# Kernel tuning notes

Hardware: AMD Instinct MI355X
Metric: run time of the kernel (lower is better)

The kernel has to match this reference:

```python
import jax, jax.numpy as jnp
import numpy as np

N, IN_DIM, H, K = 4096, 64, 64, 3
DT = 0.05


def graph_filter(z, S_powers, W):
    # z: [N, d_in], S_powers: [K, N, N], W: [K, d_in, d_out]
    zk = jnp.einsum('knm,md->knd', S_powers, z)   # K-hop diffused features
    return jnp.einsum('knd,kde->ne', zk, W)       # sum over taps k


def setup_inputs() -> dict:
    key = jax.random.key(0)
    ks = jax.random.split(key, 8)
    w_scale = 0.1
    return {
        'x': jax.random.normal(ks[0], (N, H), jnp.float32),
        'u': jax.random.normal(ks[1], (N, IN_DIM), jnp.float32),
        'S_powers': jax.random.normal(ks[2], (K, N, N), jnp.float32) / np.float32(np.sqrt(N)),
        'WA_hat': jax.random.normal(ks[3], (K, H, H), jnp.float32) * w_scale,
        'WB_hat': jax.random.normal(ks[4], (K, IN_DIM, H), jnp.float32) * w_scale,
        'WA_state': jax.random.normal(ks[5], (K, H, H), jnp.float32) * w_scale,
        'WB_state': jax.random.normal(ks[6], (K, IN_DIM, H), jnp.float32) * w_scale,
        'bx': jnp.zeros((1, H), jnp.float32),
        'bu': jnp.zeros((1, H), jnp.float32),
        'b': jnp.ones((1, H), jnp.float32) * 0.1,
        'n_steps': 4,
    }


def reference(x, u, S_powers, WA_hat, WB_hat, WA_state, WB_state, bx, bu, b, n_steps):
    # Input-driven terms are constant across solver steps; hoist them.
    fu = jax.nn.relu(graph_filter(u, S_powers, WB_hat) + bu)   # [N, H]
    sigma_c = jnp.tanh(graph_filter(u, S_powers, WB_state))    # [N, H]

    def step(xc, _):
        f = jax.nn.relu(graph_filter(xc, S_powers, WA_hat) + bx) + fu
        dx = -(b + f) * xc - graph_filter(xc, S_powers, WA_state) + f * sigma_c
        xn = jnp.clip(xc + DT * dx, -1.0, 1.0)
        return xn, None

    xf, _ = jax.lax.scan(step, x, None, length=n_steps)
    return xf
```

## Files before the change

kernel.cpp:

```cpp
#include <hip/hip_runtime.h>
#include <math.h>


typedef unsigned short u16;
typedef unsigned int u32;
typedef __attribute__((ext_vector_type(8))) short short8;
typedef __attribute__((ext_vector_type(4))) float f32x4;

#define NN 4096
#define HD 64
#define KB32 128
#define DT_C 0.05f

__device__ __forceinline__ u16 f2bf(float f) {
    u32 u = __float_as_uint(f);
    u += 0x7FFFu + ((u >> 16) & 1u);
    return (u16)(u >> 16);
}
__device__ __forceinline__ u32 pk2(float a, float b) {
    return (u32)f2bf(a) | ((u32)f2bf(b) << 16);
}

__global__ __launch_bounds__(256) void zprep_kernel(
    const float* __restrict__ u, const float* __restrict__ x,
    const float* __restrict__ WAh, const float* __restrict__ WAs,
    const float* __restrict__ WBh, const float* __restrict__ WBs,
    u16* __restrict__ utT, u16* __restrict__ xtT, u16* __restrict__ WtT)
{
    const int b = blockIdx.x;
    const int t = threadIdx.x;
    if (b < 256) {
        const float* z = (b < 128) ? u : x;
        u16* ztT = (b < 128) ? utT : xtT;
        const int kb = b & 127, n0 = kb * 32;
        __shared__ __align__(16) u16 tile[64][40];
        const int nl = t >> 3, c0 = (t & 7) * 8;
        const float* src = z + (size_t)(n0 + nl) * HD + c0;
        float4 f0 = ((const float4*)src)[0];
        float4 f1 = ((const float4*)src)[1];
        tile[c0 + 0][nl] = f2bf(f0.x); tile[c0 + 1][nl] = f2bf(f0.y);
        tile[c0 + 2][nl] = f2bf(f0.z); tile[c0 + 3][nl] = f2bf(f0.w);
        tile[c0 + 4][nl] = f2bf(f1.x); tile[c0 + 5][nl] = f2bf(f1.y);
        tile[c0 + 6][nl] = f2bf(f1.z); tile[c0 + 7][nl] = f2bf(f1.w);
        __syncthreads();
        const int e = t >> 2, kw0 = (t & 3) * 8;
        short8 v = *(const short8*)&tile[e][kw0];
        *(short8*)(ztT + ((size_t)kb * 64 + e) * 32 + kw0) = v;
    } else {
        for (int f = t; f < 4 * 6 * 64 * 32; f += 256) {
            int mat = f / 12288, r = f % 12288;
            int s = r / 2048, r2 = r % 2048;
            int e = r2 >> 5, kw = r2 & 31;
            int kp = s * 32 + kw, tap = kp >> 6, d = kp & 63;
            const float* Wm = (mat == 0) ? WAh : (mat == 1) ? WAs : (mat == 2) ? WBh : WBs;
            WtT[f] = f2bf(Wm[((size_t)tap * HD + d) * HD + e]);
        }
    }
}

__global__ __launch_bounds__(256) void diffuseA_kernel(
    const float* __restrict__ S, const u16* __restrict__ utT,
    const u16* __restrict__ xtT, u16* __restrict__ SbT,
    float* __restrict__ Yp, int iters)
{
    const int t = threadIdx.x;
    const int tap = blockIdx.z;
    const int row0 = blockIdx.x * 64;
    const int kb0 = blockIdx.y * iters;
    const int w = t >> 6, lane = t & 63, l15 = lane & 15, quad = lane >> 4;

    const int n = row0 + w * 16 + l15;
    const float* Sb = S + ((size_t)tap * NN + n) * NN + quad * 8;
    u16* Wb = SbT + (((size_t)tap * KB32) * NN + n) * 32 + quad * 8;

    f32x4 z4 = {0.f, 0.f, 0.f, 0.f};
    f32x4 acc[2][4];
    #pragma unroll
    for (int s = 0; s < 2; ++s)
        #pragma unroll
        for (int j = 0; j < 4; ++j) acc[s][j] = z4;

    #pragma unroll 2
    for (int it = 0; it < iters; ++it) {
        const int kb = kb0 + it;
        const float* sp0 = Sb + (size_t)kb * 32;
        float4 f0 = ((const float4*)sp0)[0];
        float4 f1 = ((const float4*)sp0)[1];
        short8 bu[4], bx[4];
        #pragma unroll
        for (int ct = 0; ct < 4; ++ct) {
            const size_t bo = ((size_t)kb * 64 + ct * 16 + l15) * 32 + quad * 8;
            bu[ct] = *(const short8*)(utT + bo);
            bx[ct] = *(const short8*)(xtT + bo);
        }
        union U { uint4 u4; short8 s8; };
        U A0;
        A0.u4.x = pk2(f0.x, f0.y); A0.u4.y = pk2(f0.z, f0.w);
        A0.u4.z = pk2(f1.x, f1.y); A0.u4.w = pk2(f1.z, f1.w);
        *(uint4*)(Wb + (size_t)kb * (NN * 32)) = A0.u4;
        #pragma unroll
        for (int ct = 0; ct < 4; ++ct) {
            acc[0][ct] = __builtin_amdgcn_mfma_f32_16x16x32_bf16(bu[ct], A0.s8, acc[0][ct], 0, 0, 0);
            acc[1][ct] = __builtin_amdgcn_mfma_f32_16x16x32_bf16(bx[ct], A0.s8, acc[1][ct], 0, 0, 0);
        }
    }
    #pragma unroll
    for (int s = 0; s < 2; ++s) {
        float* yb = Yp + ((size_t)((blockIdx.y * 3 + tap) * 2 + s) * NN + n) * HD + quad * 4;
        #pragma unroll
        for (int ct = 0; ct < 4; ++ct)
            *(f32x4*)(yb + ct * 16) = acc[s][ct];
    }
}

__global__ __launch_bounds__(256) void diffuseS_kernel(
    const u16* __restrict__ SbT, const u16* __restrict__ xtT,
    float* __restrict__ Yp, int iters)
{
    const int t = threadIdx.x;
    const int row0 = blockIdx.x * 64;
    const int kb0 = blockIdx.y * iters;
    const int w = t >> 6, lane = t & 63, l15 = lane & 15, quad = lane >> 4;

    const int n = row0 + w * 16 + l15;
    const u16* A0 = SbT + (size_t)n * 32 + quad * 8;
    const size_t kstr = (size_t)NN * 32;
    const size_t tstr = (size_t)KB32 * NN * 32;

    f32x4 z4 = {0.f, 0.f, 0.f, 0.f};
    f32x4 acc[3][4];
    #pragma unroll
    for (int tp = 0; tp < 3; ++tp)
        #pragma unroll
        for (int j = 0; j < 4; ++j) acc[tp][j] = z4;

    #pragma unroll 2
    for (int it = 0; it < iters; ++it) {
        const int kb = kb0 + it;
        short8 a[3];
        #pragma unroll
        for (int tp = 0; tp < 3; ++tp)
            a[tp] = *(const short8*)(A0 + (size_t)tp * tstr + (size_t)kb * kstr);
        short8 b[4];
        #pragma unroll
        for (int ct = 0; ct < 4; ++ct)
            b[ct] = *(const short8*)(xtT + ((size_t)kb * 64 + ct * 16 + l15) * 32 + quad * 8);
        #pragma unroll
        for (int tp = 0; tp < 3; ++tp)
            #pragma unroll
            for (int ct = 0; ct < 4; ++ct)
                acc[tp][ct] = __builtin_amdgcn_mfma_f32_16x16x32_bf16(b[ct], a[tp], acc[tp][ct], 0, 0, 0);
    }
    #pragma unroll
    for (int tp = 0; tp < 3; ++tp) {
        float* yb = Yp + ((size_t)(blockIdx.y * 3 + tp) * NN + n) * HD + quad * 4;
        #pragma unroll
        for (int ct = 0; ct < 4; ++ct)
            *(f32x4*)(yb + ct * 16) = acc[tp][ct];
    }
}

__global__ __launch_bounds__(256) void update_step_kernel(
    const float* __restrict__ Yp, int KS, const u16* __restrict__ WtT,
    const float* __restrict__ bx, const float* __restrict__ bvec,
    const float* __restrict__ fu, const float* __restrict__ sc,
    const float* __restrict__ xc, float* __restrict__ xn,
    u16* __restrict__ xtT, int do_pack)
{
    __shared__ __align__(16) u16 yt[6][16][56];
    __shared__ __align__(16) u16 pkt[64][24];
    const int t = threadIdx.x;
    const int n0 = blockIdx.x * 16;

    for (int f = t; f < 384; f += 256) {
        const int tap = f >> 7;
        const int r = f & 127;
        const int nl = r >> 3, d8 = r & 7, d0 = d8 * 8;
        const float* p = Yp + ((size_t)tap * NN + n0 + nl) * HD + d0;
        const size_t kstride = (size_t)3 * NN * HD;
        float4 s0 = {0.f, 0.f, 0.f, 0.f}, s1 = {0.f, 0.f, 0.f, 0.f};
        for (int y = 0; y < KS; ++y) {
            float4 v0 = ((const float4*)(p + (size_t)y * kstride))[0];
            float4 v1 = ((const float4*)(p + (size_t)y * kstride))[1];
            s0.x += v0.x; s0.y += v0.y; s0.z += v0.z; s0.w += v0.w;
            s1.x += v1.x; s1.y += v1.y; s1.z += v1.z; s1.w += v1.w;
        }
        uint4 o;
        o.x = pk2(s0.x, s0.y); o.y = pk2(s0.z, s0.w);
        o.z = pk2(s1.x, s1.y); o.w = pk2(s1.z, s1.w);
        const int s = tap * 2 + (d8 >> 2), kw0 = (d8 & 3) * 8;
        *(uint4*)&yt[s][nl][kw0] = o;
    }
    __syncthreads();

    const int wv = t >> 6, lane = t & 63, l15 = lane & 15, quad = lane >> 4;
    f32x4 z4 = {0.f, 0.f, 0.f, 0.f};
    f32x4 aF = z4, aG = z4;
    #pragma unroll
    for (int s = 0; s < 6; ++s) {
        short8 a = *(const short8*)&yt[s][l15][quad * 8];
        const size_t wo = ((size_t)s * 64 + wv * 16 + l15) * 32 + quad * 8;
        short8 bF = *(const short8*)(WtT + wo);
        short8 bG = *(const short8*)(WtT + wo + 12288);
        aF = __builtin_amdgcn_mfma_f32_16x16x32_bf16(a, bF, aF, 0, 0, 0);
        aG = __builtin_amdgcn_mfma_f32_16x16x32_bf16(a, bG, aG, 0, 0, 0);
    }
    const int e = wv * 16 + l15;
    const float bxv = bx[e], bbv = bvec[e];
    float xos[4];
    #pragma unroll
    for (int r = 0; r < 4; ++r) {
        const int n = n0 + quad * 4 + r;
        const size_t o = (size_t)n * HD + e;
        float ff = fmaxf(aF[r] + bxv, 0.f) + fu[o];
        float xv = xc[o];
        float dx = -(bbv + ff) * xv - aG[r] + ff * sc[o];
        float xo = fminf(fmaxf(xv + DT_C * dx, -1.f), 1.f);
        xn[o] = xo;
        xos[r] = xo;
    }
    if (do_pack) {
        uint2 pv;
        pv.x = pk2(xos[0], xos[1]);
        pv.y = pk2(xos[2], xos[3]);
        *(uint2*)&pkt[e][quad * 4] = pv;
        __syncthreads();
        if (t < 128) {
            const int ee = t >> 1, g = t & 1;
            short8 v = *(const short8*)&pkt[ee][g * 8];
            const int kb = n0 >> 5;
            const int kwb = (n0 & 31) + g * 8;
            *(short8*)(xtT + ((size_t)kb * 64 + ee) * 32 + kwb) = v;
        }
    }
}

__global__ __launch_bounds__(256) void update1_kernel(
    const float* __restrict__ Yp, int KS, const u16* __restrict__ WtT,
    const float* __restrict__ bx, const float* __restrict__ bu,
    const float* __restrict__ bvec, const float* __restrict__ x0,
    float* __restrict__ fu, float* __restrict__ sc, float* __restrict__ x1,
    u16* __restrict__ xtT)
{
    __shared__ __align__(16) u16 yt[2][6][16][56];
    __shared__ __align__(16) u16 pkt[64][24];
    const int t = threadIdx.x;
    const int n0 = blockIdx.x * 16;

    #pragma unroll
    for (int ff = 0; ff < 3; ++ff) {
        const int f = t + ff * 256;
        const int src = f / 384;
        const int r3 = f - src * 384;
        const int tap = r3 >> 7;
        const int r = r3 & 127;
        const int nl = r >> 3, d8 = r & 7, d0 = d8 * 8;
        const float* p = Yp + (((size_t)(tap * 2 + src)) * NN + n0 + nl) * HD + d0;
        const size_t kstride = (size_t)6 * NN * HD;
        float4 s0 = {0.f, 0.f, 0.f, 0.f}, s1 = {0.f, 0.f, 0.f, 0.f};
        for (int y = 0; y < KS; ++y) {
            float4 v0 = ((const float4*)(p + (size_t)y * kstride))[0];
            float4 v1 = ((const float4*)(p + (size_t)y * kstride))[1];
            s0.x += v0.x; s0.y += v0.y; s0.z += v0.z; s0.w += v0.w;
            s1.x += v1.x; s1.y += v1.y; s1.z += v1.z; s1.w += v1.w;
        }
        uint4 o;
        o.x = pk2(s0.x, s0.y); o.y = pk2(s0.z, s0.w);
        o.z = pk2(s1.x, s1.y); o.w = pk2(s1.z, s1.w);
        const int s = tap * 2 + (d8 >> 2), kw0 = (d8 & 3) * 8;
        *(uint4*)&yt[src][s][nl][kw0] = o;
    }
    __syncthreads();

    const int wv = t >> 6, lane = t & 63, l15 = lane & 15, quad = lane >> 4;
    f32x4 z4 = {0.f, 0.f, 0.f, 0.f};
    f32x4 aF = z4, aG = z4, aFu = z4, aSc = z4;
    #pragma unroll
    for (int s = 0; s < 6; ++s) {
        short8 au = *(const short8*)&yt[0][s][l15][quad * 8];
        short8 ax = *(const short8*)&yt[1][s][l15][quad * 8];
        const size_t wo = ((size_t)s * 64 + wv * 16 + l15) * 32 + quad * 8;
        short8 bF  = *(const short8*)(WtT + wo);
        short8 bG  = *(const short8*)(WtT + wo + 12288);
        short8 bFu = *(const short8*)(WtT + wo + 2 * 12288);
        short8 bSc = *(const short8*)(WtT + wo + 3 * 12288);
        aF  = __builtin_amdgcn_mfma_f32_16x16x32_bf16(ax, bF,  aF,  0, 0, 0);
        aG  = __builtin_amdgcn_mfma_f32_16x16x32_bf16(ax, bG,  aG,  0, 0, 0);
        aFu = __builtin_amdgcn_mfma_f32_16x16x32_bf16(au, bFu, aFu, 0, 0, 0);
        aSc = __builtin_amdgcn_mfma_f32_16x16x32_bf16(au, bSc, aSc, 0, 0, 0);
    }
    const int e = wv * 16 + l15;
    const float bxv = bx[e], buv = bu[e], bbv = bvec[e];
    float xos[4];
    #pragma unroll
    for (int r = 0; r < 4; ++r) {
        const int n = n0 + quad * 4 + r;
        const size_t o = (size_t)n * HD + e;
        float fuv = fmaxf(aFu[r] + buv, 0.f);
        float scv = tanhf(aSc[r]);
        float ff = fmaxf(aF[r] + bxv, 0.f) + fuv;
        float xv = x0[o];
        float dx = -(bbv + ff) * xv - aG[r] + ff * scv;
        float xo = fminf(fmaxf(xv + DT_C * dx, -1.f), 1.f);
        fu[o] = fuv; sc[o] = scv; x1[o] = xo;
        xos[r] = xo;
    }
    {
        uint2 pv;
        pv.x = pk2(xos[0], xos[1]);
        pv.y = pk2(xos[2], xos[3]);
        *(uint2*)&pkt[e][quad * 4] = pv;
        __syncthreads();
        if (t < 128) {
            const int ee = t >> 1, g = t & 1;
            short8 v = *(const short8*)&pkt[ee][g * 8];
            const int kb = n0 >> 5;
            const int kwb = (n0 & 31) + g * 8;
            *(short8*)(xtT + ((size_t)kb * 64 + ee) * 32 + kwb) = v;
        }
    }
}

extern "C" void kernel_launch(void* const* d_in, const int* in_sizes, int n_in,
                              void* d_out, int out_size, void* d_ws, size_t ws_size,
                              hipStream_t stream) {
    const float* x   = (const float*)d_in[0];
    const float* u   = (const float*)d_in[1];
    const float* S   = (const float*)d_in[2];
    const float* WAh = (const float*)d_in[3];
    const float* WBh = (const float*)d_in[4];
    const float* WAs = (const float*)d_in[5];
    const float* WBs = (const float*)d_in[6];
    const float* bx  = (const float*)d_in[7];
    const float* bu  = (const float*)d_in[8];
    const float* bvec= (const float*)d_in[9];
    float* out = (float*)d_out;

    const size_t sbf_bytes = (size_t)3 * NN * NN * 2;
    const size_t slice = (size_t)NN * HD * 4;
    const size_t rest = 2 * 524288 + 98304 + 4 * 1048576;
    int KS_A = 8, KS_S = 16;
    if (ws_size < sbf_bytes + 48 * slice + rest) { KS_A = 4; KS_S = 8; }
    if (ws_size < sbf_bytes + 24 * slice + rest) { KS_A = 2; KS_S = 4; }
    if (ws_size < sbf_bytes + 12 * slice + rest) { KS_A = 1; KS_S = 2; }
    const int nslice = (KS_A * 6 > KS_S * 3) ? KS_A * 6 : KS_S * 3;

    char* p = (char*)d_ws;
    u16* SbT  = (u16*)p;         p += sbf_bytes;
    float* Yp = (float*)p;       p += (size_t)nslice * slice;
    u16* utT  = (u16*)p;         p += 524288;
    u16* xtT  = (u16*)p;         p += 524288;
    u16* WtT  = (u16*)p;         p += 98304;
    float* fu = (float*)p;       p += 1048576;
    float* sc = (float*)p;       p += 1048576;
    float* xA = (float*)p;       p += 1048576;
    float* xB = (float*)p;       p += 1048576;

    zprep_kernel<<<257, 256, 0, stream>>>(u, x, WAh, WAs, WBh, WBs, utT, xtT, WtT);

    diffuseA_kernel<<<dim3(64, KS_A, 3), 256, 0, stream>>>(S, utT, xtT, SbT, Yp, KB32 / KS_A);
    update1_kernel<<<256, 256, 0, stream>>>(Yp, KS_A, WtT, bx, bu, bvec, x, fu, sc, xA, xtT);

    diffuseS_kernel<<<dim3(64, KS_S), 256, 0, stream>>>(SbT, xtT, Yp, KB32 / KS_S);
    update_step_kernel<<<256, 256, 0, stream>>>(Yp, KS_S, WtT, bx, bvec, fu, sc, xA, xB, xtT, 1);

    diffuseS_kernel<<<dim3(64, KS_S), 256, 0, stream>>>(SbT, xtT, Yp, KB32 / KS_S);
    update_step_kernel<<<256, 256, 0, stream>>>(Yp, KS_S, WtT, bx, bvec, fu, sc, xB, xA, xtT, 1);

    diffuseS_kernel<<<dim3(64, KS_S), 256, 0, stream>>>(SbT, xtT, Yp, KB32 / KS_S);
    update_step_kernel<<<256, 256, 0, stream>>>(Yp, KS_S, WtT, bx, bvec, fu, sc, xA, out, xtT, 0);
}
```

Measured before the change: 520.8 us.

## Split diffuseS across taps in grid z, template split-K reduction, shrink split factors

The S-diffusion kernel now gives each tap its own block via blockIdx.z instead of looping over three taps per block. This cuts accumulator registers and raises block count, and the loop is unrolled by two. The split-K factors drop from 8/16 to 4/8, which halves the partial-sum workspace and the reduction traffic in the update kernels. Those kernels now take KS as a template parameter so their reduction loops fully unroll. In exchange, each tap block reloads the same x tiles, so x operand loads are tripled.

```diff
diff --git a/kernel.cpp b/kernel.cpp
--- a/kernel.cpp
+++ b/kernel.cpp
@@ -118,50 +118,46 @@
     float* __restrict__ Yp, int iters)
 {
     const int t = threadIdx.x;
+    const int tap = blockIdx.z;
     const int row0 = blockIdx.x * 64;
     const int kb0 = blockIdx.y * iters;
     const int w = t >> 6, lane = t & 63, l15 = lane & 15, quad = lane >> 4;
 
     const int n = row0 + w * 16 + l15;
-    const u16* A0 = SbT + (size_t)n * 32 + quad * 8;
+    const u16* A0 = SbT + (((size_t)(tap * KB32)) * NN + n) * 32 + quad * 8;
     const size_t kstr = (size_t)NN * 32;
-    const size_t tstr = (size_t)KB32 * NN * 32;
 
     f32x4 z4 = {0.f, 0.f, 0.f, 0.f};
-    f32x4 acc[3][4];
-    #pragma unroll
-    for (int tp = 0; tp < 3; ++tp)
-        #pragma unroll
-        for (int j = 0; j < 4; ++j) acc[tp][j] = z4;
-
-    #pragma unroll 2
-    for (int it = 0; it < iters; ++it) {
-        const int kb = kb0 + it;
-        short8 a[3];
-        #pragma unroll
-        for (int tp = 0; tp < 3; ++tp)
-            a[tp] = *(const short8*)(A0 + (size_t)tp * tstr + (size_t)kb * kstr);
-        short8 b[4];
-        #pragma unroll
-        for (int ct = 0; ct < 4; ++ct)
-            b[ct] = *(const short8*)(xtT + ((size_t)kb * 64 + ct * 16 + l15) * 32 + quad * 8);
-        #pragma unroll
-        for (int tp = 0; tp < 3; ++tp)
+    f32x4 acc[4];
+    #pragma unroll
+    for (int j = 0; j < 4; ++j) acc[j] = z4;
+
+    for (int it0 = 0; it0 < iters; it0 += 2) {
+        short8 a[2];
+        short8 b[2][4];
+        #pragma unroll
+        for (int j = 0; j < 2; ++j) {
+            const int kb = kb0 + it0 + j;
+            a[j] = *(const short8*)(A0 + (size_t)kb * kstr);
             #pragma unroll
             for (int ct = 0; ct < 4; ++ct)
-                acc[tp][ct] = __builtin_amdgcn_mfma_f32_16x16x32_bf16(b[ct], a[tp], acc[tp][ct], 0, 0, 0);
-    }
-    #pragma unroll
-    for (int tp = 0; tp < 3; ++tp) {
-        float* yb = Yp + ((size_t)(blockIdx.y * 3 + tp) * NN + n) * HD + quad * 4;
-        #pragma unroll
-        for (int ct = 0; ct < 4; ++ct)
-            *(f32x4*)(yb + ct * 16) = acc[tp][ct];
-    }
-}
-
+                b[j][ct] = *(const short8*)(xtT + ((size_t)kb * 64 + ct * 16 + l15) * 32 + quad * 8);
+        }
+        #pragma unroll
+        for (int j = 0; j < 2; ++j)
+            #pragma unroll
+            for (int ct = 0; ct < 4; ++ct)
+                acc[ct] = __builtin_amdgcn_mfma_f32_16x16x32_bf16(b[j][ct], a[j], acc[ct], 0, 0, 0);
+    }
+    float* yb = Yp + ((size_t)(blockIdx.y * 3 + tap) * NN + n) * HD + quad * 4;
+    #pragma unroll
+    for (int ct = 0; ct < 4; ++ct)
+        *(f32x4*)(yb + ct * 16) = acc[ct];
+}
+
+template<int KS>
 __global__ __launch_bounds__(256) void update_step_kernel(
-    const float* __restrict__ Yp, int KS, const u16* __restrict__ WtT,
+    const float* __restrict__ Yp, const u16* __restrict__ WtT,
     const float* __restrict__ bx, const float* __restrict__ bvec,
     const float* __restrict__ fu, const float* __restrict__ sc,
     const float* __restrict__ xc, float* __restrict__ xn,
@@ -179,6 +175,7 @@
         const float* p = Yp + ((size_t)tap * NN + n0 + nl) * HD + d0;
         const size_t kstride = (size_t)3 * NN * HD;
         float4 s0 = {0.f, 0.f, 0.f, 0.f}, s1 = {0.f, 0.f, 0.f, 0.f};
+        #pragma unroll
         for (int y = 0; y < KS; ++y) {
             float4 v0 = ((const float4*)(p + (size_t)y * kstride))[0];
             float4 v1 = ((const float4*)(p + (size_t)y * kstride))[1];
@@ -235,8 +232,9 @@
     }
 }
 
+template<int KS>
 __global__ __launch_bounds__(256) void update1_kernel(
-    const float* __restrict__ Yp, int KS, const u16* __restrict__ WtT,
+    const float* __restrict__ Yp, const u16* __restrict__ WtT,
     const float* __restrict__ bx, const float* __restrict__ bu,
     const float* __restrict__ bvec, const float* __restrict__ x0,
     float* __restrict__ fu, float* __restrict__ sc, float* __restrict__ x1,
@@ -258,6 +256,7 @@
         const float* p = Yp + (((size_t)(tap * 2 + src)) * NN + n0 + nl) * HD + d0;
         const size_t kstride = (size_t)6 * NN * HD;
         float4 s0 = {0.f, 0.f, 0.f, 0.f}, s1 = {0.f, 0.f, 0.f, 0.f};
+        #pragma unroll
         for (int y = 0; y < KS; ++y) {
             float4 v0 = ((const float4*)(p + (size_t)y * kstride))[0];
             float4 v1 = ((const float4*)(p + (size_t)y * kstride))[1];
@@ -339,11 +338,10 @@
     const size_t sbf_bytes = (size_t)3 * NN * NN * 2;
     const size_t slice = (size_t)NN * HD * 4;
     const size_t rest = 2 * 524288 + 98304 + 4 * 1048576;
-    int KS_A = 8, KS_S = 16;
-    if (ws_size < sbf_bytes + 48 * slice + rest) { KS_A = 4; KS_S = 8; }
-    if (ws_size < sbf_bytes + 24 * slice + rest) { KS_A = 2; KS_S = 4; }
-    if (ws_size < sbf_bytes + 12 * slice + rest) { KS_A = 1; KS_S = 2; }
-    const int nslice = (KS_A * 6 > KS_S * 3) ? KS_A * 6 : KS_S * 3;
+    int tier = 0;
+    if (ws_size < sbf_bytes + 24 * slice + rest) tier = 1;
+    if (ws_size < sbf_bytes + 12 * slice + rest) tier = 2;
+    const int nslice = (tier == 0) ? 24 : (tier == 1) ? 12 : 6;
 
     char* p = (char*)d_ws;
     u16* SbT  = (u16*)p;         p += sbf_bytes;
@@ -358,15 +356,25 @@
 
     zprep_kernel<<<257, 256, 0, stream>>>(u, x, WAh, WAs, WBh, WBs, utT, xtT, WtT);
 
-    diffuseA_kernel<<<dim3(64, KS_A, 3), 256, 0, stream>>>(S, utT, xtT, SbT, Yp, KB32 / KS_A);
-    update1_kernel<<<256, 256, 0, stream>>>(Yp, KS_A, WtT, bx, bu, bvec, x, fu, sc, xA, xtT);
-
-    diffuseS_kernel<<<dim3(64, KS_S), 256, 0, stream>>>(SbT, xtT, Yp, KB32 / KS_S);
-    update_step_kernel<<<256, 256, 0, stream>>>(Yp, KS_S, WtT, bx, bvec, fu, sc, xA, xB, xtT, 1);
-
-    diffuseS_kernel<<<dim3(64, KS_S), 256, 0, stream>>>(SbT, xtT, Yp, KB32 / KS_S);
-    update_step_kernel<<<256, 256, 0, stream>>>(Yp, KS_S, WtT, bx, bvec, fu, sc, xB, xA, xtT, 1);
-
-    diffuseS_kernel<<<dim3(64, KS_S), 256, 0, stream>>>(SbT, xtT, Yp, KB32 / KS_S);
-    update_step_kernel<<<256, 256, 0, stream>>>(Yp, KS_S, WtT, bx, bvec, fu, sc, xA, out, xtT, 0);
-}
+#define RUN_PIPE(KA, KSs)                                                                   \
+    do {                                                                                    \
+        diffuseA_kernel<<<dim3(64, KA, 3), 256, 0, stream>>>(S, utT, xtT, SbT, Yp,          \
+                                                             KB32 / (KA));                  \
+        update1_kernel<KA><<<256, 256, 0, stream>>>(Yp, WtT, bx, bu, bvec, x, fu, sc, xA,   \
+                                                    xtT);                                   \
+        diffuseS_kernel<<<dim3(64, KSs, 3), 256, 0, stream>>>(SbT, xtT, Yp, KB32 / (KSs));  \
+        update_step_kernel<KSs><<<256, 256, 0, stream>>>(Yp, WtT, bx, bvec, fu, sc, xA, xB, \
+                                                         xtT, 1);                           \
+        diffuseS_kernel<<<dim3(64, KSs, 3), 256, 0, stream>>>(SbT, xtT, Yp, KB32 / (KSs));  \
+        update_step_kernel<KSs><<<256, 256, 0, stream>>>(Yp, WtT, bx, bvec, fu, sc, xB, xA, \
+                                                         xtT, 1);                           \
+        diffuseS_kernel<<<dim3(64, KSs, 3), 256, 0, stream>>>(SbT, xtT, Yp, KB32 / (KSs));  \
+        update_step_kernel<KSs><<<256, 256, 0, stream>>>(Yp, WtT, bx, bvec, fu, sc, xA,     \
+                                                         out, xtT, 0);                      \
+    } while (0)
+
+    if (tier == 0)      RUN_PIPE(4, 8);
+    else if (tier == 1) RUN_PIPE(2, 4);
+    else                RUN_PIPE(1, 2);
+#undef RUN_PIPE
+}
```

After: 523.3 us. No clear change (+0.5%).
